# Optimization experiments

Hardware: AMD Instinct MI355X
Metric: run time of the kernel (lower is better)

Reference implementation:

```python
import jax, jax.numpy as jnp
import numpy as np
from jax import lax


def setup_inputs() -> dict:
    key = jax.random.key(0)
    k1, k2, k3 = jax.random.split(key, 3)
    x = jax.random.normal(k1, (16, 32, 48, 48, 48), dtype=jnp.float32)
    w = jax.random.normal(k2, (64, 32, 3, 3, 3), dtype=jnp.float32) * 0.05
    b = jax.random.normal(k3, (64,), dtype=jnp.float32) * 0.05
    return {"x": x, "w": w, "b": b}


def reference(x, w, b):
    # conv3d, stride=1, padding=1 (NCDHW / OIDHW)
    y = lax.conv_general_dilated(
        x, w,
        window_strides=(1, 1, 1),
        padding=[(1, 1), (1, 1), (1, 1)],
        dimension_numbers=("NCDHW", "OIDHW", "NCDHW"),
    )
    y = y + b[None, :, None, None, None]  # [N, Cout, 48, 48, 48]
    # maxpool3d kernel=2 stride=2 (ceil_mode=False)
    y = lax.reduce_window(
        y, -jnp.inf, lax.max,
        window_dimensions=(1, 1, 2, 2, 2),
        window_strides=(1, 1, 2, 2, 2),
        padding="VALID",
    )  # [N, Cout, 24, 24, 24]
    # logsumexp over channel dim (keepdim), then ReLU
    lse = jax.nn.logsumexp(y, axis=1, keepdims=True)  # [N, 1, 24, 24, 24]
    return jnp.maximum(lse, 0.0)
```

## Files before the change

kernel.cpp:

```cpp
#include <hip/hip_runtime.h>
#include <math.h>

#define CIN 32
#define COUT 64
#define DIM 48
#define PD 24
#define D3 110592

typedef __bf16 bf16x8 __attribute__((ext_vector_type(8)));
typedef float f32x4 __attribute__((ext_vector_type(4)));

__device__ __forceinline__ unsigned bf16_rne(float f) {
    unsigned u = __builtin_bit_cast(unsigned, f);
    return (u + 0x7fffu + ((u >> 16) & 1u)) >> 16;
}

__global__ __launch_bounds__(256) void wpack_kernel(const float* __restrict__ w,
                                                    unsigned short* __restrict__ wg) {
    int i = blockIdx.x * 256 + threadIdx.x;
    if (i >= 27 * 64 * 32) return;
    int cin = i & 31, cout = (i >> 5) & 63, tap = i >> 11;
    float v = w[(cout * CIN + cin) * 27 + tap];
    wg[i] = (unsigned short)bf16_rne(v);
}

__global__ __launch_bounds__(256, 3) void conv_mfma_kernel(
    const float* __restrict__ x, const unsigned short* __restrict__ wg,
    const float* __restrict__ bias, float* __restrict__ out)
{
    __shared__ __align__(16) unsigned short xs[648 * 40];

    const int tid = threadIdx.x;
    const int bw = blockIdx.x % 3;
    const int bh = (blockIdx.x / 3) % 12;
    const int bd = (blockIdx.x / 36) % 12;
    const int n  = blockIdx.x / 432;
    const int d0 = bd * 4 - 1, h0 = bh * 4 - 1, w0 = bw * 16 - 1;

    const float* xn = x + (size_t)n * CIN * D3;
    {
        const int cp = tid >> 4;
        const int sl = tid & 15;
        const float* xp0 = xn + (size_t)(cp * 2) * D3;
        for (int itb = 0; itb < 6; ++itb) {
            float f0[8], f1[8];
            int sv[8];
#pragma unroll
            for (int u = 0; u < 8; ++u) {
                const int s = sl + ((itb * 8 + u) << 4);
                sv[u] = s;
                f0[u] = 0.f; f1[u] = 0.f;
                if (s < 648) {
                    const int lw = s % 18, t = s / 18, lh = t % 6, ld = t / 6;
                    const int gd = d0 + ld, gh = h0 + lh, gw = w0 + lw;
                    if ((unsigned)gd < 48u && (unsigned)gh < 48u && (unsigned)gw < 48u) {
                        const float* p = xp0 + (gd * DIM + gh) * DIM + gw;
                        f0[u] = p[0];
                        f1[u] = p[D3];
                    }
                }
            }
#pragma unroll
            for (int u = 0; u < 8; ++u)
                if (sv[u] < 648)
                    ((unsigned*)xs)[sv[u] * 20 + cp] =
                        bf16_rne(f0[u]) | (bf16_rne(f1[u]) << 16);
        }
    }

    const int lane = tid & 63;
    const int wv = tid >> 6;
    const int m  = lane & 15;
    const int ch = lane >> 4;

    const unsigned short* wgp = wg + m * 32 + ch * 8;

    bf16x8 bcur[4], bnxt[4];
#pragma unroll
    for (int nt = 0; nt < 4; ++nt)
        bcur[nt] = *(const bf16x8*)(wgp + nt * 512);

    __syncthreads();

    f32x4 acc[4][4];
#pragma unroll
    for (int i = 0; i < 4; ++i)
#pragma unroll
        for (int j = 0; j < 4; ++j)
            acc[i][j] = (f32x4)0.f;

#pragma unroll
    for (int tap = 0; tap < 27; ++tap) {
        if (tap < 26) {
#pragma unroll
            for (int nt = 0; nt < 4; ++nt)
                bnxt[nt] = *(const bf16x8*)(wgp + (tap + 1) * 2048 + nt * 512);
        }
        const int kd = tap / 9, kh = (tap / 3) % 3, kw = tap % 3;
        bf16x8 af[4];
#pragma unroll
        for (int hz = 0; hz < 4; ++hz) {
            const int row = ((wv + kd) * 6 + (hz + kh)) * 18 + (m + kw);
            af[hz] = *(const bf16x8*)(xs + row * 40 + ch * 8);
        }
#pragma unroll
        for (int hz = 0; hz < 4; ++hz)
#pragma unroll
            for (int nt = 0; nt < 4; ++nt)
                acc[hz][nt] = __builtin_amdgcn_mfma_f32_16x16x32_bf16(
                    af[hz], bcur[nt], acc[hz][nt], 0, 0, 0);
#pragma unroll
        for (int nt = 0; nt < 4; ++nt) bcur[nt] = bnxt[nt];
    }
    __syncthreads();

    float* pmax = (float*)xs;
#pragma unroll
    for (int ph = 0; ph < 2; ++ph)
#pragma unroll
        for (int b = 0; b < 2; ++b)
#pragma unroll
            for (int nt = 0; nt < 4; ++nt) {
                float v = fmaxf(
                    fmaxf(acc[2 * ph][nt][2 * b], acc[2 * ph][nt][2 * b + 1]),
                    fmaxf(acc[2 * ph + 1][nt][2 * b], acc[2 * ph + 1][nt][2 * b + 1]));
                int pw = 2 * ch + b;
                pmax[((wv * 2 + ph) * 8 + pw) * 64 + nt * 16 + m] = v;
            }
    __syncthreads();

    float* pooled = pmax + 4096;
    for (int v = tid; v < 2048; v += 256) {
        int c = v & 63, cell = v >> 6;
        int pd = cell >> 4, ph = (cell >> 3) & 1, pw = cell & 7;
        int i1 = ((4 * pd + ph) * 8 + pw) * 64 + c;
        pooled[cell * 65 + c] = fmaxf(pmax[i1], pmax[i1 + 1024]) + bias[c];
    }
    __syncthreads();

    if (tid < 32) {
        int pd = tid >> 4, ph = (tid >> 3) & 1, pw = tid & 7;
        float mx = -INFINITY;
        for (int c = 0; c < 64; ++c) mx = fmaxf(mx, pooled[tid * 65 + c]);
        float s = 0.f;
        for (int c = 0; c < 64; ++c) s += __expf(pooled[tid * 65 + c] - mx);
        float r = fmaxf(mx + __logf(s), 0.f);
        int od = bd * 2 + pd, oh = bh * 2 + ph, ow = bw * 8 + pw;
        out[((size_t)(n * PD + od) * PD + oh) * PD + ow] = r;
    }
}

__global__ __launch_bounds__(256) void conv_fused_fallback(
    const float* __restrict__ x, const float* __restrict__ wsrc,
    const float* __restrict__ bias, float* __restrict__ out)
{
    __shared__ float smem[CIN * 216];
    const int tid = threadIdx.x;
    const int bid = blockIdx.x;
    const int tw = bid % 12, th = (bid / 12) % 12, td = (bid / 144) % 12, n = bid / 1728;
    const int d0 = td * 4, h0 = th * 4, w0 = tw * 4;
    const float* xn = x + (size_t)n * CIN * D3;
    for (int i = tid; i < CIN * 216; i += 256) {
        int cin = i / 216, r = i % 216;
        int dz = r / 36, hz = (r / 6) % 6, wz = r % 6;
        int gd = d0 - 1 + dz, gh = h0 - 1 + hz, gw = w0 - 1 + wz;
        float v = 0.f;
        if ((unsigned)gd < 48u && (unsigned)gh < 48u && (unsigned)gw < 48u)
            v = xn[((cin * DIM + gd) * DIM + gh) * DIM + gw];
        smem[i] = v;
    }
    __syncthreads();
    const int lane = tid & 63;
    const int wv = __builtin_amdgcn_readfirstlane(tid >> 6);
    const int cout0 = wv * 16;
    const int ld = lane >> 4, lh = (lane >> 2) & 3, lw = lane & 3;
    float acc[16];
#pragma unroll
    for (int c = 0; c < 16; ++c) acc[c] = 0.f;
    for (int cin = 0; cin < CIN; ++cin) {
        const int xb = cin * 216 + ld * 36 + lh * 6 + lw;
#pragma unroll
        for (int kd = 0; kd < 3; ++kd)
#pragma unroll
            for (int kh = 0; kh < 3; ++kh)
#pragma unroll
                for (int kw = 0; kw < 3; ++kw) {
                    const float xv = smem[xb + kd * 36 + kh * 6 + kw];
                    const int tap = (kd * 3 + kh) * 3 + kw;
#pragma unroll
                    for (int c = 0; c < 16; ++c)
                        acc[c] = fmaf(xv, wsrc[((cout0 + c) * CIN + cin) * 27 + tap], acc[c]);
                }
    }
    __syncthreads();
    float* cb = smem;
#pragma unroll
    for (int c = 0; c < 16; ++c) cb[(wv * 64 + lane) * 16 + c] = acc[c];
    __syncthreads();
    float* pool = smem + 4096;
    for (int v = tid; v < 512; v += 256) {
        const int pp = v >> 6, c = v & 63;
        const int pd = pp >> 2, ph = (pp >> 1) & 1, pw = pp & 1;
        float mv = -INFINITY;
#pragma unroll
        for (int i = 0; i < 2; ++i)
#pragma unroll
            for (int j = 0; j < 2; ++j)
#pragma unroll
                for (int k = 0; k < 2; ++k) {
                    const int l = ((2 * pd + i) << 4) | ((2 * ph + j) << 2) | (2 * pw + k);
                    mv = fmaxf(mv, cb[((c >> 4) * 64 + l) * 16 + (c & 15)]);
                }
        pool[pp * 64 + c] = mv + bias[c];
    }
    __syncthreads();
    if (tid < 8) {
        float mx = -INFINITY;
        for (int c = 0; c < 64; ++c) mx = fmaxf(mx, pool[tid * 64 + c]);
        float s = 0.f;
        for (int c = 0; c < 64; ++c) s += __expf(pool[tid * 64 + c] - mx);
        float r = fmaxf(mx + logf(s), 0.f);
        const int pd = tid >> 2, ph = (tid >> 1) & 1, pw = tid & 1;
        const int dp = td * 2 + pd, hp = th * 2 + ph, wp = tw * 2 + pw;
        out[(((size_t)n * PD + dp) * PD + hp) * PD + wp] = r;
    }
}

extern "C" void kernel_launch(void* const* d_in, const int* in_sizes, int n_in,
                              void* d_out, int out_size, void* d_ws, size_t ws_size,
                              hipStream_t stream) {
    const float* x = (const float*)d_in[0];
    const float* w = (const float*)d_in[1];
    const float* b = (const float*)d_in[2];
    float* out = (float*)d_out;

    if (ws_size >= (size_t)(27 * 64 * 32) * sizeof(unsigned short)) {
        unsigned short* wgb = (unsigned short*)d_ws;
        wpack_kernel<<<216, 256, 0, stream>>>(w, wgb);
        conv_mfma_kernel<<<16 * 12 * 12 * 3, 256, 0, stream>>>(x, wgb, b, out);
    } else {
        conv_fused_fallback<<<16 * 12 * 12 * 12, 256, 0, stream>>>(x, w, b, out);
    }
}
```

Baseline: 552.6 us.

## Prepack input into padded channels-last bf16 buffer before the MFMA conv

A new pre-pass kernel converts x into a zero-padded (50^3) channels-last bf16 workspace buffer. The conv kernel then fills its shared-memory tile with 16-byte vector loads and no bounds checks or per-element conversion. The old on-the-fly conversion path is kept as a separate kernel for smaller workspaces. In exchange, the change needs a 128 MB workspace and an extra full read of x plus a write of the packed copy on every call.

```diff
diff --git a/kernel.cpp b/kernel.cpp
--- a/kernel.cpp
+++ b/kernel.cpp
@@ -6,6 +6,10 @@
 #define DIM 48
 #define PD 24
 #define D3 110592
+
+#define XP_W 50
+#define XP_POS 125000
+#define XB_BYTES 128000000ull
 
 typedef __bf16 bf16x8 __attribute__((ext_vector_type(8)));
 typedef float f32x4 __attribute__((ext_vector_type(4)));
@@ -24,8 +28,34 @@
     wg[i] = (unsigned short)bf16_rne(v);
 }
 
+__global__ __launch_bounds__(256) void xpack_kernel(const float* __restrict__ x,
+                                                    unsigned short* __restrict__ xb) {
+    int i = blockIdx.x * 256 + threadIdx.x;
+    if (i >= 16 * XP_POS) return;
+    int pw = i % 50, t = i / 50, ph = t % 50, t2 = t / 50, pd = t2 % 50, n = t2 / 50;
+    uint4* dst = (uint4*)(xb + (size_t)i * 32);
+    int gd = pd - 1, gh = ph - 1, gw = pw - 1;
+    if ((unsigned)gd < 48u && (unsigned)gh < 48u && (unsigned)gw < 48u) {
+        const float* p = x + (size_t)n * CIN * D3 + ((size_t)gd * DIM + gh) * DIM + gw;
+        unsigned pk[16];
+#pragma unroll
+        for (int cp = 0; cp < 16; ++cp) {
+            float a = p[(size_t)(2 * cp) * D3];
+            float b = p[(size_t)(2 * cp + 1) * D3];
+            pk[cp] = bf16_rne(a) | (bf16_rne(b) << 16);
+        }
+#pragma unroll
+        for (int q = 0; q < 4; ++q)
+            dst[q] = make_uint4(pk[4 * q], pk[4 * q + 1], pk[4 * q + 2], pk[4 * q + 3]);
+    } else {
+        uint4 z = make_uint4(0, 0, 0, 0);
+#pragma unroll
+        for (int q = 0; q < 4; ++q) dst[q] = z;
+    }
+}
+
 __global__ __launch_bounds__(256, 3) void conv_mfma_kernel(
-    const float* __restrict__ x, const unsigned short* __restrict__ wg,
+    const unsigned short* __restrict__ xb, const unsigned short* __restrict__ wg,
     const float* __restrict__ bias, float* __restrict__ out)
 {
     __shared__ __align__(16) unsigned short xs[648 * 40];
@@ -35,36 +65,27 @@
     const int bh = (blockIdx.x / 3) % 12;
     const int bd = (blockIdx.x / 36) % 12;
     const int n  = blockIdx.x / 432;
-    const int d0 = bd * 4 - 1, h0 = bh * 4 - 1, w0 = bw * 16 - 1;
-
-    const float* xn = x + (size_t)n * CIN * D3;
-    {
-        const int cp = tid >> 4;
-        const int sl = tid & 15;
-        const float* xp0 = xn + (size_t)(cp * 2) * D3;
-        for (int itb = 0; itb < 6; ++itb) {
-            float f0[8], f1[8];
-            int sv[8];
-#pragma unroll
-            for (int u = 0; u < 8; ++u) {
-                const int s = sl + ((itb * 8 + u) << 4);
-                sv[u] = s;
-                f0[u] = 0.f; f1[u] = 0.f;
-                if (s < 648) {
-                    const int lw = s % 18, t = s / 18, lh = t % 6, ld = t / 6;
-                    const int gd = d0 + ld, gh = h0 + lh, gw = w0 + lw;
-                    if ((unsigned)gd < 48u && (unsigned)gh < 48u && (unsigned)gw < 48u) {
-                        const float* p = xp0 + (gd * DIM + gh) * DIM + gw;
-                        f0[u] = p[0];
-                        f1[u] = p[D3];
-                    }
-                }
-            }
-#pragma unroll
-            for (int u = 0; u < 8; ++u)
-                if (sv[u] < 648)
-                    ((unsigned*)xs)[sv[u] * 20 + cp] =
-                        bf16_rne(f0[u]) | (bf16_rne(f1[u]) << 16);
+
+    const unsigned short* xtile = xb + (size_t)n * (XP_POS * 32)
+                                + (size_t)(bd * 4) * (2500 * 32)
+                                + (bh * 4) * (50 * 32) + (bw * 16) * 32;
+
+    uint4 stg[11];
+#pragma unroll
+    for (int it = 0; it < 11; ++it) {
+        int qq = tid + it * 256;
+        if (qq < 2592) {
+            int row = qq >> 2, c = qq & 3;
+            int lw = row % 18, t = row / 18, lh = t % 6, ld = t / 6;
+            stg[it] = *(const uint4*)(xtile + (size_t)ld * 80000 + lh * 1600 + lw * 32 + c * 8);
+        }
+    }
+#pragma unroll
+    for (int it = 0; it < 11; ++it) {
+        int qq = tid + it * 256;
+        if (qq < 2592) {
+            int row = qq >> 2, c = qq & 3;
+            *(uint4*)((char*)xs + row * 80 + c * 16) = stg[it];
         }
     }
 
@@ -138,6 +159,113 @@
     }
     __syncthreads();
 
+    if (tid < 32) {
+        int pd = tid >> 4, ph = (tid >> 3) & 1, pw = tid & 7;
+        float mx = -INFINITY;
+        for (int c = 0; c < 64; ++c) mx = fmaxf(mx, pooled[tid * 65 + c]);
+        float s = 0.f;
+        for (int c = 0; c < 64; ++c) s += __expf(pooled[tid * 65 + c] - mx);
+        float r = fmaxf(mx + __logf(s), 0.f);
+        int od = bd * 2 + pd, oh = bh * 2 + ph, ow = bw * 8 + pw;
+        out[((size_t)(n * PD + od) * PD + oh) * PD + ow] = r;
+    }
+}
+
+__global__ __launch_bounds__(256, 3) void conv_mfma_r3(
+    const float* __restrict__ x, const unsigned short* __restrict__ wg,
+    const float* __restrict__ bias, float* __restrict__ out)
+{
+    __shared__ __align__(16) unsigned short xs[648 * 40];
+    const int tid = threadIdx.x;
+    const int bw = blockIdx.x % 3;
+    const int bh = (blockIdx.x / 3) % 12;
+    const int bd = (blockIdx.x / 36) % 12;
+    const int n  = blockIdx.x / 432;
+    const int d0 = bd * 4 - 1, h0 = bh * 4 - 1, w0 = bw * 16 - 1;
+    const float* xn = x + (size_t)n * CIN * D3;
+    {
+        const int cp = tid >> 4, sl = tid & 15;
+        const float* xp0 = xn + (size_t)(cp * 2) * D3;
+        for (int itb = 0; itb < 6; ++itb) {
+            float f0[8], f1[8];
+            int sv[8];
+#pragma unroll
+            for (int u = 0; u < 8; ++u) {
+                const int s = sl + ((itb * 8 + u) << 4);
+                sv[u] = s; f0[u] = 0.f; f1[u] = 0.f;
+                if (s < 648) {
+                    const int lw = s % 18, t = s / 18, lh = t % 6, ld = t / 6;
+                    const int gd = d0 + ld, gh = h0 + lh, gw = w0 + lw;
+                    if ((unsigned)gd < 48u && (unsigned)gh < 48u && (unsigned)gw < 48u) {
+                        const float* p = xp0 + (gd * DIM + gh) * DIM + gw;
+                        f0[u] = p[0]; f1[u] = p[D3];
+                    }
+                }
+            }
+#pragma unroll
+            for (int u = 0; u < 8; ++u)
+                if (sv[u] < 648)
+                    ((unsigned*)xs)[sv[u] * 20 + cp] = bf16_rne(f0[u]) | (bf16_rne(f1[u]) << 16);
+        }
+    }
+    const int lane = tid & 63;
+    const int wv = tid >> 6;
+    const int m  = lane & 15;
+    const int ch = lane >> 4;
+    const unsigned short* wgp = wg + m * 32 + ch * 8;
+    bf16x8 bcur[4], bnxt[4];
+#pragma unroll
+    for (int nt = 0; nt < 4; ++nt) bcur[nt] = *(const bf16x8*)(wgp + nt * 512);
+    __syncthreads();
+    f32x4 acc[4][4];
+#pragma unroll
+    for (int i = 0; i < 4; ++i)
+#pragma unroll
+        for (int j = 0; j < 4; ++j) acc[i][j] = (f32x4)0.f;
+#pragma unroll
+    for (int tap = 0; tap < 27; ++tap) {
+        if (tap < 26) {
+#pragma unroll
+            for (int nt = 0; nt < 4; ++nt)
+                bnxt[nt] = *(const bf16x8*)(wgp + (tap + 1) * 2048 + nt * 512);
+        }
+        const int kd = tap / 9, kh = (tap / 3) % 3, kw = tap % 3;
+        bf16x8 af[4];
+#pragma unroll
+        for (int hz = 0; hz < 4; ++hz) {
+            const int row = ((wv + kd) * 6 + (hz + kh)) * 18 + (m + kw);
+            af[hz] = *(const bf16x8*)(xs + row * 40 + ch * 8);
+        }
+#pragma unroll
+        for (int hz = 0; hz < 4; ++hz)
+#pragma unroll
+            for (int nt = 0; nt < 4; ++nt)
+                acc[hz][nt] = __builtin_amdgcn_mfma_f32_16x16x32_bf16(af[hz], bcur[nt], acc[hz][nt], 0, 0, 0);
+#pragma unroll
+        for (int nt = 0; nt < 4; ++nt) bcur[nt] = bnxt[nt];
+    }
+    __syncthreads();
+    float* pmax = (float*)xs;
+#pragma unroll
+    for (int ph = 0; ph < 2; ++ph)
+#pragma unroll
+        for (int b = 0; b < 2; ++b)
+#pragma unroll
+            for (int nt = 0; nt < 4; ++nt) {
+                float v = fmaxf(fmaxf(acc[2 * ph][nt][2 * b], acc[2 * ph][nt][2 * b + 1]),
+                                fmaxf(acc[2 * ph + 1][nt][2 * b], acc[2 * ph + 1][nt][2 * b + 1]));
+                int pw = 2 * ch + b;
+                pmax[((wv * 2 + ph) * 8 + pw) * 64 + nt * 16 + m] = v;
+            }
+    __syncthreads();
+    float* pooled = pmax + 4096;
+    for (int v = tid; v < 2048; v += 256) {
+        int c = v & 63, cell = v >> 6;
+        int pd = cell >> 4, ph = (cell >> 3) & 1, pw = cell & 7;
+        int i1 = ((4 * pd + ph) * 8 + pw) * 64 + c;
+        pooled[cell * 65 + c] = fmaxf(pmax[i1], pmax[i1 + 1024]) + bias[c];
+    }
+    __syncthreads();
     if (tid < 32) {
         int pd = tid >> 4, ph = (tid >> 3) & 1, pw = tid & 7;
         float mx = -INFINITY;
@@ -178,14 +306,14 @@
 #pragma unroll
     for (int c = 0; c < 16; ++c) acc[c] = 0.f;
     for (int cin = 0; cin < CIN; ++cin) {
-        const int xb = cin * 216 + ld * 36 + lh * 6 + lw;
+        const int xb2 = cin * 216 + ld * 36 + lh * 6 + lw;
 #pragma unroll
         for (int kd = 0; kd < 3; ++kd)
 #pragma unroll
             for (int kh = 0; kh < 3; ++kh)
 #pragma unroll
                 for (int kw = 0; kw < 3; ++kw) {
-                    const float xv = smem[xb + kd * 36 + kh * 6 + kw];
+                    const float xv = smem[xb2 + kd * 36 + kh * 6 + kw];
                     const int tap = (kd * 3 + kh) * 3 + kw;
 #pragma unroll
                     for (int c = 0; c < 16; ++c)
@@ -234,10 +362,17 @@
     const float* b = (const float*)d_in[2];
     float* out = (float*)d_out;
 
-    if (ws_size >= (size_t)(27 * 64 * 32) * sizeof(unsigned short)) {
+    const size_t wg_bytes = (size_t)(27 * 64 * 32) * sizeof(unsigned short);
+    if (ws_size >= XB_BYTES + wg_bytes) {
+        unsigned short* xbuf = (unsigned short*)d_ws;
+        unsigned short* wgb  = (unsigned short*)((char*)d_ws + XB_BYTES);
+        xpack_kernel<<<(16 * XP_POS + 255) / 256, 256, 0, stream>>>(x, xbuf);
+        wpack_kernel<<<216, 256, 0, stream>>>(w, wgb);
+        conv_mfma_kernel<<<16 * 12 * 12 * 3, 256, 0, stream>>>(xbuf, wgb, b, out);
+    } else if (ws_size >= wg_bytes) {
         unsigned short* wgb = (unsigned short*)d_ws;
         wpack_kernel<<<216, 256, 0, stream>>>(w, wgb);
-        conv_mfma_kernel<<<16 * 12 * 12 * 3, 256, 0, stream>>>(x, wgb, b, out);
+        conv_mfma_r3<<<16 * 12 * 12 * 3, 256, 0, stream>>>(x, wgb, b, out);
     } else {
         conv_fused_fallback<<<16 * 12 * 12 * 12, 256, 0, stream>>>(x, w, b, out);
     }
```

Measured after the change: 594.5 us. 7.6% more time.
